# Performance work log

Hardware: AMD Instinct MI355X
Metric: run time of the kernel (lower is better)

The kernel has to match this reference:

```python
import jax, jax.numpy as jnp
import numpy as np

TOP_K = 8
N_EXPERTS = 64
ALPHA = 0.001
EPS = 1e-9


def setup_inputs() -> dict:
    key = jax.random.key(0)
    k1, k2 = jax.random.split(key)
    B, S, H, E = 4, 4096, 2048, N_EXPERTS
    hidden_states = jax.random.normal(k1, (B, S, H), dtype=jnp.float32)
    # kaiming_uniform_(a=sqrt(5)) on [E,H] -> bound = 1/sqrt(H)
    bound = 1.0 / np.sqrt(H)
    weight = jax.random.uniform(k2, (E, H), dtype=jnp.float32, minval=-bound, maxval=bound)
    return {"hidden_states": hidden_states, "weight": weight}


def reference(hidden_states, weight):
    B, S, H = hidden_states.shape
    E = weight.shape[0]
    x = hidden_states.reshape(-1, H)                     # [N, H], N = B*S
    logits = jnp.einsum('nh,eh->ne', x, weight)          # [N, E]
    scores = jax.nn.sigmoid(logits)                      # sigmoid affinity (DeepSeek-V3 style)

    topk_weight, topk_idx = jax.lax.top_k(scores, TOP_K)  # [N, K]
    # norm_topk_prob = True and top_k > 1
    denom = topk_weight.sum(axis=-1, keepdims=True) + EPS
    topk_weight = topk_weight / denom

    # aux load-balance loss (training, alpha > 0); scatter-count instead of one_hot
    N = x.shape[0]
    counts = jnp.zeros((E,), dtype=jnp.float32).at[topk_idx.reshape(-1)].add(1.0)
    load = counts / (N * TOP_K)                          # == one_hot.mean(dim=(0,1))
    prob_raw = scores / (scores.sum(axis=-1, keepdims=True) + EPS)
    prob = prob_raw.mean(axis=0)
    prob = prob / (prob.sum() + EPS)
    aux_loss = ALPHA * (load * prob).sum() * E

    return topk_idx, topk_weight, aux_loss
```

## Files before the change

kernel.cpp:

```cpp
#include <hip/hip_runtime.h>
#include <math.h>

#define N_TOK 16384
#define HDIM  2048
#define NEXP  64
#define TOPK  8
#define NKS   4
#define KSEG  (HDIM / NKS)
#define KCH   32
#define NCH   (KSEG / KCH)

#define PART_OFF  0
#define STATS_OFF (33u << 20)

typedef double d4 __attribute__((ext_vector_type(4)));

__global__ void mfma_probe_kernel(int* __restrict__ flag) {
    const int l = threadIdx.x;
    const int i16 = l & 15, q = l >> 4;
    const int r4 = l >> 2,  m4 = l & 3;
    int fv = 0;
#pragma unroll
    for (int ai = 0; ai < 2; ++ai)
#pragma unroll
    for (int bi = 0; bi < 2; ++bi) {
        const int ra = ai ? r4 : i16, ka = ai ? m4 : q;
        const int cb = bi ? r4 : i16, kb = bi ? m4 : q;
        double a = (double)(ra * 4 + ka + 1);
        double b = (double)((kb + 1) * 100 + 3 * cb);
        d4 acc = {0., 0., 0., 0.};
        acc = __builtin_amdgcn_mfma_f64_16x16x4f64(a, b, acc, 0, 0, 0);
#pragma unroll
        for (int sf = 0; sf < 2; ++sf)
#pragma unroll
        for (int tr = 0; tr < 2; ++tr) {
            int ok = 1;
#pragma unroll
            for (int r = 0; r < 4; ++r) {
                const int p   = sf ? (q + 4 * r) : (4 * q + r);
                const int row = tr ? i16 : p;
                const int col = tr ? p : i16;
                double ref = 0.0;
#pragma unroll
                for (int k = 0; k < 4; ++k)
                    ref += (double)(row * 4 + k + 1) * (double)((k + 1) * 100 + 3 * col);
                ok &= (acc[r] == ref);
            }
            if (__all(ok) && fv == 0) fv = 1 + ai * 8 + bi * 4 + sf * 2 + tr;
        }
    }
    if (l == 0) *flag = fv;
}

__global__ __launch_bounds__(256) void gemm_mfma_kernel(const float* __restrict__ X,
                                                        const float* __restrict__ W,
                                                        const int* __restrict__ flag,
                                                        double* __restrict__ part) {
    const int f = *flag;
    if (f == 0) return;
    const int fb = f - 1;
    const int ai = (fb >> 3) & 1, bi = (fb >> 2) & 1;
    const int sf = (fb >> 1) & 1, tr = fb & 1;

    const int tt  = blockIdx.x >> 2;
    const int ks  = blockIdx.x & 3;
    const int tid = threadIdx.x;
    const int l   = tid & 63;
    const int wv  = tid >> 6;
    const int wr  = wv >> 1, wc = wv & 1;
    const int tok0 = tt * 64;
    const int k0   = ks * KSEG;

    const int i16 = l & 15, q = l >> 4, r4 = l >> 2, m4 = l & 3;
    const int ra = ai ? r4 : i16, ka = ai ? m4 : q;
    const int cb = bi ? r4 : i16, kb = bi ? m4 : q;

    __shared__ double Xs[64][34];
    __shared__ double Ws[64][34];

    d4 acc[2][2];
#pragma unroll
    for (int i = 0; i < 2; ++i)
#pragma unroll
        for (int j = 0; j < 2; ++j) acc[i][j] = (d4){0., 0., 0., 0.};

    const int rs = tid >> 2, cu = tid & 3;
    const float* xg = X + (size_t)(tok0 + rs) * HDIM + k0 + cu;
    const float* wg = W + (size_t)rs * HDIM + k0 + cu;

    float fx[8], fw[8];
#pragma unroll
    for (int j = 0; j < 4; ++j) {
        fx[2 * j]     = xg[8 * j];
        fx[2 * j + 1] = xg[8 * j + 4];
        fw[2 * j]     = wg[8 * j];
        fw[2 * j + 1] = wg[8 * j + 4];
    }

    for (int c = 0; c < NCH; ++c) {
        __syncthreads();
#pragma unroll
        for (int j = 0; j < 4; ++j) {
            double2 dx; dx.x = (double)fx[2 * j]; dx.y = (double)fx[2 * j + 1];
            double2 dw; dw.x = (double)fw[2 * j]; dw.y = (double)fw[2 * j + 1];
            *(double2*)&Xs[rs][8 * cu + 2 * j] = dx;
            *(double2*)&Ws[rs][8 * cu + 2 * j] = dw;
        }
        __syncthreads();
        if (c + 1 < NCH) {
            const float* xn = xg + (c + 1) * KCH;
            const float* wn = wg + (c + 1) * KCH;
#pragma unroll
            for (int j = 0; j < 4; ++j) {
                fx[2 * j]     = xn[8 * j];
                fx[2 * j + 1] = xn[8 * j + 4];
                fw[2 * j]     = wn[8 * j];
                fw[2 * j + 1] = wn[8 * j + 4];
            }
        }
        const double* pa0 = &Xs[wr * 32 + ra][8 * ka];
        const double* pa1 = &Xs[wr * 32 + 16 + ra][8 * ka];
        const double* pb0 = &Ws[wc * 32 + cb][8 * kb];
        const double* pb1 = &Ws[wc * 32 + 16 + cb][8 * kb];
#pragma unroll
        for (int t = 0; t < 4; ++t) {
            double2 a0 = *(const double2*)(pa0 + 2 * t);
            double2 a1 = *(const double2*)(pa1 + 2 * t);
            double2 b0 = *(const double2*)(pb0 + 2 * t);
            double2 b1 = *(const double2*)(pb1 + 2 * t);
            acc[0][0] = __builtin_amdgcn_mfma_f64_16x16x4f64(a0.x, b0.x, acc[0][0], 0, 0, 0);
            acc[0][1] = __builtin_amdgcn_mfma_f64_16x16x4f64(a0.x, b1.x, acc[0][1], 0, 0, 0);
            acc[1][0] = __builtin_amdgcn_mfma_f64_16x16x4f64(a1.x, b0.x, acc[1][0], 0, 0, 0);
            acc[1][1] = __builtin_amdgcn_mfma_f64_16x16x4f64(a1.x, b1.x, acc[1][1], 0, 0, 0);
            acc[0][0] = __builtin_amdgcn_mfma_f64_16x16x4f64(a0.y, b0.y, acc[0][0], 0, 0, 0);
            acc[0][1] = __builtin_amdgcn_mfma_f64_16x16x4f64(a0.y, b1.y, acc[0][1], 0, 0, 0);
            acc[1][0] = __builtin_amdgcn_mfma_f64_16x16x4f64(a1.y, b0.y, acc[1][0], 0, 0, 0);
            acc[1][1] = __builtin_amdgcn_mfma_f64_16x16x4f64(a1.y, b1.y, acc[1][1], 0, 0, 0);
        }
    }

    double* pbase = part + (size_t)ks * N_TOK * NEXP;
#pragma unroll
    for (int rt = 0; rt < 2; ++rt)
#pragma unroll
        for (int ct = 0; ct < 2; ++ct)
#pragma unroll
            for (int r = 0; r < 4; ++r) {
                const int p    = sf ? (q + 4 * r) : (4 * q + r);
                const int dtok = tr ? i16 : p;
                const int dex  = tr ? p : i16;
                const int tok  = tok0 + wr * 32 + rt * 16 + dtok;
                const int ex   = wc * 32 + ct * 16 + dex;
                pbase[(size_t)tok * NEXP + ex] = acc[rt][ct][r];
            }
}

__global__ __launch_bounds__(512, 4) void gemm_valu_kernel(const float* __restrict__ X,
                                                           const float* __restrict__ W,
                                                           const int* __restrict__ flag,
                                                           double* __restrict__ part) {
    if (*flag != 0) return;
    const int tt   = blockIdx.x >> 2;
    const int ks   = blockIdx.x & 3;
    const int tid  = threadIdx.x;
    const int lane = tid & 63;
    const int wv   = tid >> 6;
    const int tok0 = tt * 64;
    const int k0   = ks * KSEG;

    __shared__ double xs[64][18];
    __shared__ double wsh[16][66];

    double acc[8];
#pragma unroll
    for (int t = 0; t < 8; ++t) acc[t] = 0.0;

    const int sx_tok = tid >> 3;
    const int sx_k   = (tid & 7) * 2;
    const float* xg  = X + (size_t)(tok0 + sx_tok) * HDIM + k0 + sx_k;
    const int sw_k = tid >> 5;
    const int sw_e = (tid & 31) * 2;
    const float* wg0 = W + (size_t)sw_e * HDIM + k0 + sw_k;
    const float* wg1 = W + (size_t)(sw_e + 1) * HDIM + k0 + sw_k;

    float2 px = *(const float2*)xg;
    float  pa = *wg0, pb2 = *wg1;

    for (int c = 0; c < KSEG / 16; ++c) {
        __syncthreads();
        {
            double2 xv; xv.x = (double)px.x; xv.y = (double)px.y;
            *(double2*)&xs[sx_tok][sx_k] = xv;
            double2 wv2; wv2.x = (double)pa; wv2.y = (double)pb2;
            *(double2*)&wsh[sw_k][sw_e] = wv2;
        }
        __syncthreads();
        if (c + 1 < KSEG / 16) {
            px  = *(const float2*)(xg + (c + 1) * 16);
            pa  = wg0[(c + 1) * 16];
            pb2 = wg1[(c + 1) * 16];
        }
        double wr_[16];
#pragma unroll
        for (int j = 0; j < 16; ++j) wr_[j] = wsh[j][lane];
#pragma unroll
        for (int t = 0; t < 8; ++t) {
            const int trr = wv * 8 + t;
#pragma unroll
            for (int kp = 0; kp < 8; ++kp) {
                double2 xv = *(const double2*)&xs[trr][kp * 2];
                acc[t] = fma(xv.x, wr_[kp * 2],     acc[t]);
                acc[t] = fma(xv.y, wr_[kp * 2 + 1], acc[t]);
            }
        }
    }

    double* pb = part + ((size_t)ks * N_TOK + tok0 + wv * 8) * NEXP + lane;
#pragma unroll
    for (int t = 0; t < 8; ++t)
        pb[(size_t)t * NEXP] = acc[t];
}

__global__ __launch_bounds__(256) void topk_kernel(const double* __restrict__ part,
                                                   float* __restrict__ outIdx,
                                                   float* __restrict__ outW,
                                                   float* __restrict__ stats) {
    __shared__ float sc_s[32][65];
    __shared__ float lds_counts[NEXP];
    __shared__ float psum_part[4][NEXP];
    const int tid  = threadIdx.x;
    const int lane = tid & 63;
    const int w    = tid >> 6;
    if (tid < NEXP) lds_counts[tid] = 0.f;

    const int t0 = blockIdx.x * 32;
#pragma unroll
    for (int p = 0; p < 8; ++p) {
        const int idx = p * 256 + tid;
        const int t   = idx >> 6;
        const int e   = idx & 63;
        const double* pp = part + ((size_t)(t0 + t)) * NEXP + e;
        double l = (pp[0] + pp[(size_t)N_TOK * NEXP]) +
                   (pp[2 * (size_t)N_TOK * NEXP] + pp[3 * (size_t)N_TOK * NEXP]);
        sc_s[t][e] = (float)(1.0 / (1.0 + exp(-l)));
    }
    __syncthreads();

    float ps = 0.f;
    for (int i = 0; i < 8; ++i) {
        const int tloc = w * 8 + i;
        const int t    = t0 + tloc;
        float s = sc_s[tloc][lane];

        float rs = s;
#pragma unroll
        for (int off = 32; off; off >>= 1) rs += __shfl_xor(rs, off);
        ps += s / (rs + 1e-9f);

        float cur = s;
        float denom = 0.f;
        int   wi = 0;
        float wvv = 0.f;
#pragma unroll
        for (int k = 0; k < TOPK; ++k) {
            float m = cur; int mi = lane;
#pragma unroll
            for (int off = 32; off; off >>= 1) {
                float om = __shfl_xor(m, off);
                int   oi = __shfl_xor(mi, off);
                if (om > m || (om == m && oi < mi)) { m = om; mi = oi; }
            }
            denom += m;
            if (lane == k)  { wi = mi; wvv = m; }
            if (lane == mi) cur = -1e30f;
        }
        if (lane < TOPK) {
            outIdx[(size_t)t * TOPK + lane] = (float)wi;
            outW  [(size_t)t * TOPK + lane] = wvv / (denom + 1e-9f);
            atomicAdd(&lds_counts[wi], 1.f);
        }
    }
    psum_part[w][lane] = ps;
    __syncthreads();
    if (tid < NEXP) {
        float tot = psum_part[0][tid] + psum_part[1][tid] +
                    psum_part[2][tid] + psum_part[3][tid];
        atomicAdd(&stats[tid], tot);
        atomicAdd(&stats[NEXP + tid], lds_counts[tid]);
    }
}

__global__ void aux_kernel(const float* __restrict__ stats, float* __restrict__ out) {
    const int e = threadIdx.x;
    float prob = stats[e] / (float)N_TOK;
    float cnt  = stats[NEXP + e];
    float loadf = cnt / ((float)N_TOK * TOPK);
    float S = prob;
#pragma unroll
    for (int off = 32; off; off >>= 1) S += __shfl_xor(S, off);
    float pn = prob / (S + 1e-9f);
    float v  = loadf * pn;
#pragma unroll
    for (int off = 32; off; off >>= 1) v += __shfl_xor(v, off);
    if (e == 0) out[2 * N_TOK * TOPK] = 0.001f * v * (float)NEXP;
}

extern "C" void kernel_launch(void* const* d_in, const int* in_sizes, int n_in,
                              void* d_out, int out_size, void* d_ws, size_t ws_size,
                              hipStream_t stream) {
    (void)in_sizes; (void)n_in; (void)out_size; (void)ws_size;
    const float* X = (const float*)d_in[0];
    const float* W = (const float*)d_in[1];
    float* out = (float*)d_out;
    char*  ws  = (char*)d_ws;
    double* part  = (double*)(ws + PART_OFF);
    float*  stats = (float*)(ws + STATS_OFF);
    int*    flag  = (int*)(stats + 128);

    hipMemsetAsync(stats, 0, 132 * sizeof(float), stream);
    mfma_probe_kernel<<<1, 64, 0, stream>>>(flag);
    gemm_mfma_kernel<<<1024, 256, 0, stream>>>(X, W, flag, part);
    gemm_valu_kernel<<<1024, 512, 0, stream>>>(X, W, flag, part);
    topk_kernel<<<512, 256, 0, stream>>>(part, out, out + N_TOK * TOPK, stats);
    aux_kernel<<<1, 64, 0, stream>>>(stats, out);
}
```

Baseline: 154.0 us.

## Load MFMA operands directly from global memory, dropping LDS staging

```diff
diff --git a/kernel.cpp b/kernel.cpp
--- a/kernel.cpp
+++ b/kernel.cpp
@@ -7,8 +7,6 @@
 #define TOPK  8
 #define NKS   4
 #define KSEG  (HDIM / NKS)
-#define KCH   32
-#define NCH   (KSEG / KCH)
 
 #define PART_OFF  0
 #define STATS_OFF (33u << 20)
@@ -75,75 +73,37 @@
     const int ra = ai ? r4 : i16, ka = ai ? m4 : q;
     const int cb = bi ? r4 : i16, kb = bi ? m4 : q;
 
-    __shared__ double Xs[64][34];
-    __shared__ double Ws[64][34];
-
-    d4 acc[2][2];
-#pragma unroll
-    for (int i = 0; i < 2; ++i)
-#pragma unroll
-        for (int j = 0; j < 2; ++j) acc[i][j] = (d4){0., 0., 0., 0.};
-
-    const int rs = tid >> 2, cu = tid & 3;
-    const float* xg = X + (size_t)(tok0 + rs) * HDIM + k0 + cu;
-    const float* wg = W + (size_t)rs * HDIM + k0 + cu;
-
-    float fx[8], fw[8];
-#pragma unroll
-    for (int j = 0; j < 4; ++j) {
-        fx[2 * j]     = xg[8 * j];
-        fx[2 * j + 1] = xg[8 * j + 4];
-        fw[2 * j]     = wg[8 * j];
-        fw[2 * j + 1] = wg[8 * j + 4];
-    }
-
-    for (int c = 0; c < NCH; ++c) {
-        __syncthreads();
-#pragma unroll
-        for (int j = 0; j < 4; ++j) {
-            double2 dx; dx.x = (double)fx[2 * j]; dx.y = (double)fx[2 * j + 1];
-            double2 dw; dw.x = (double)fw[2 * j]; dw.y = (double)fw[2 * j + 1];
-            *(double2*)&Xs[rs][8 * cu + 2 * j] = dx;
-            *(double2*)&Ws[rs][8 * cu + 2 * j] = dw;
-        }
-        __syncthreads();
-        if (c + 1 < NCH) {
-            const float* xn = xg + (c + 1) * KCH;
-            const float* wn = wg + (c + 1) * KCH;
-#pragma unroll
-            for (int j = 0; j < 4; ++j) {
-                fx[2 * j]     = xn[8 * j];
-                fx[2 * j + 1] = xn[8 * j + 4];
-                fw[2 * j]     = wn[8 * j];
-                fw[2 * j + 1] = wn[8 * j + 4];
-            }
-        }
-        const double* pa0 = &Xs[wr * 32 + ra][8 * ka];
-        const double* pa1 = &Xs[wr * 32 + 16 + ra][8 * ka];
-        const double* pb0 = &Ws[wc * 32 + cb][8 * kb];
-        const double* pb1 = &Ws[wc * 32 + 16 + cb][8 * kb];
-#pragma unroll
-        for (int t = 0; t < 4; ++t) {
-            double2 a0 = *(const double2*)(pa0 + 2 * t);
-            double2 a1 = *(const double2*)(pa1 + 2 * t);
-            double2 b0 = *(const double2*)(pb0 + 2 * t);
-            double2 b1 = *(const double2*)(pb1 + 2 * t);
-            acc[0][0] = __builtin_amdgcn_mfma_f64_16x16x4f64(a0.x, b0.x, acc[0][0], 0, 0, 0);
-            acc[0][1] = __builtin_amdgcn_mfma_f64_16x16x4f64(a0.x, b1.x, acc[0][1], 0, 0, 0);
-            acc[1][0] = __builtin_amdgcn_mfma_f64_16x16x4f64(a1.x, b0.x, acc[1][0], 0, 0, 0);
-            acc[1][1] = __builtin_amdgcn_mfma_f64_16x16x4f64(a1.x, b1.x, acc[1][1], 0, 0, 0);
-            acc[0][0] = __builtin_amdgcn_mfma_f64_16x16x4f64(a0.y, b0.y, acc[0][0], 0, 0, 0);
-            acc[0][1] = __builtin_amdgcn_mfma_f64_16x16x4f64(a0.y, b1.y, acc[0][1], 0, 0, 0);
-            acc[1][0] = __builtin_amdgcn_mfma_f64_16x16x4f64(a1.y, b0.y, acc[1][0], 0, 0, 0);
-            acc[1][1] = __builtin_amdgcn_mfma_f64_16x16x4f64(a1.y, b1.y, acc[1][1], 0, 0, 0);
-        }
+    const float* xa0 = X + (size_t)(tok0 + wr * 32 + ra) * HDIM + k0 + ka;
+    const float* xa1 = xa0 + (size_t)16 * HDIM;
+    const float* wb0 = W + (size_t)(wc * 32 + cb) * HDIM + k0 + kb;
+    const float* wb1 = wb0 + (size_t)16 * HDIM;
+
+    d4 acc00 = {0., 0., 0., 0.};
+    d4 acc01 = {0., 0., 0., 0.};
+    d4 acc10 = {0., 0., 0., 0.};
+    d4 acc11 = {0., 0., 0., 0.};
+
+#pragma unroll 8
+    for (int kq = 0; kq < KSEG / 4; ++kq) {
+        float fa0 = xa0[4 * kq];
+        float fa1 = xa1[4 * kq];
+        float fb0 = wb0[4 * kq];
+        float fb1 = wb1[4 * kq];
+        double a0 = (double)fa0, a1 = (double)fa1;
+        double b0 = (double)fb0, b1 = (double)fb1;
+        acc00 = __builtin_amdgcn_mfma_f64_16x16x4f64(a0, b0, acc00, 0, 0, 0);
+        acc01 = __builtin_amdgcn_mfma_f64_16x16x4f64(a0, b1, acc01, 0, 0, 0);
+        acc10 = __builtin_amdgcn_mfma_f64_16x16x4f64(a1, b0, acc10, 0, 0, 0);
+        acc11 = __builtin_amdgcn_mfma_f64_16x16x4f64(a1, b1, acc11, 0, 0, 0);
     }
 
     double* pbase = part + (size_t)ks * N_TOK * NEXP;
 #pragma unroll
     for (int rt = 0; rt < 2; ++rt)
 #pragma unroll
-        for (int ct = 0; ct < 2; ++ct)
+        for (int ct = 0; ct < 2; ++ct) {
+            const d4 accv = rt == 0 ? (ct == 0 ? acc00 : acc01)
+                                    : (ct == 0 ? acc10 : acc11);
 #pragma unroll
             for (int r = 0; r < 4; ++r) {
                 const int p    = sf ? (q + 4 * r) : (4 * q + r);
@@ -151,8 +111,9 @@
                 const int dex  = tr ? p : i16;
                 const int tok  = tok0 + wr * 32 + rt * 16 + dtok;
                 const int ex   = wc * 32 + ct * 16 + dex;
-                pbase[(size_t)tok * NEXP + ex] = acc[rt][ct][r];
-            }
+                pbase[(size_t)tok * NEXP + ex] = accv[r];
+            }
+        }
 }
 
 __global__ __launch_bounds__(512, 4) void gemm_valu_kernel(const float* __restrict__ X,
```

Result: slower. 294.8 us (+91.4%).
